# Kernel tuning notes

Hardware: AMD Instinct MI355X
Metric: run time of the kernel (lower is better)

The kernel has to match this reference:

```python
import jax, jax.numpy as jnp
import numpy as np

B, T, L, D, S = 256, 64, 32, 128, 4


def setup_inputs() -> dict:
    key = jax.random.key(0)
    k0, k1, k2, k3, k4, k5 = jax.random.split(key, 6)
    X = jax.random.normal(k0, (B, T, D), jnp.float32)
    decoding_manifold_means = jax.random.normal(k1, (B, S, T, D), jnp.float32)
    R_diag = jax.random.uniform(k2, (D,), jnp.float32, 0.5, 1.5)
    encoding_mus = jax.random.normal(k3, (B, T, L), jnp.float32)
    # PSD per-latent posterior covariance blocks: Sigma = 0.01*A A^T + I
    A = jax.random.normal(k4, (B, L, T, T), jnp.float32) * 0.1
    Sig = A @ jnp.swapaxes(A, -1, -2) + jnp.eye(T, dtype=jnp.float32)  # [B,L,T,T]
    encoding_Sigmas = jnp.transpose(Sig, (0, 2, 3, 1))  # [B,T,T,L]
    # RBF GP prior kernel per latent with noise jitter (sde_kernel_matrices analogue)
    times = jnp.arange(T, dtype=jnp.float32)
    taus = jax.random.uniform(k5, (L,), jnp.float32, 2.0, 10.0)
    dt2 = (times[:, None] - times[None, :]) ** 2  # [T,T]
    signal_var, noise_var = 0.999, 1e-3
    K = signal_var * jnp.exp(-dt2[:, :, None] / (2.0 * taus[None, None, :] ** 2))
    K = K + noise_var * jnp.eye(T, dtype=jnp.float32)[:, :, None]  # [T,T,L]
    return {
        "X": X,
        "decoding_manifold_means": decoding_manifold_means,
        "R_diag": R_diag,
        "encoding_mus": encoding_mus,
        "encoding_Sigmas": encoding_Sigmas,
        "K": K,
    }


def _gpml_loss(X, decoding_manifold_means, R_diag, encoding_mus, encoding_Sigmas, K):
    Bx, Tt, Ld = encoding_mus.shape
    Dd = X.shape[-1]
    # ---- KL(q || prior), exploiting block-diagonal structure over latents ----
    Sig = jnp.transpose(encoding_Sigmas, (0, 3, 1, 2))  # [B,L,T,T]
    Kp = jnp.transpose(K, (2, 0, 1))                    # [L,T,T]
    Lk = jnp.linalg.cholesky(Kp)                        # [L,T,T]
    Ls = jnp.linalg.cholesky(Sig)                       # [B,L,T,T]
    logdet_K = 2.0 * jnp.sum(jnp.log(jnp.diagonal(Lk, axis1=-2, axis2=-1)), -1)  # [L]
    logdet_S = 2.0 * jnp.sum(jnp.log(jnp.diagonal(Ls, axis1=-2, axis2=-1)), -1)  # [B,L]
    # tr(K^-1 Sigma) = ||Lk^-1 Ls||_F^2
    M = jax.scipy.linalg.solve_triangular(Lk[None], Ls, lower=True)  # [B,L,T,T]
    trace_term = jnp.sum(M * M, axis=(-2, -1))                       # [B,L]
    mu = jnp.transpose(encoding_mus, (0, 2, 1))                      # [B,L,T]
    w = jax.scipy.linalg.solve_triangular(Lk[None], mu[..., None], lower=True)  # [B,L,T,1]
    maha = jnp.sum(w * w, axis=(-2, -1))                             # [B,L]
    kl = 0.5 * jnp.sum(logdet_K[None, :] - logdet_S - Tt + trace_term + maha, axis=1)  # [B]
    # ---- log-likelihood under diagonal-R Gaussian observation model ----
    diff = X[:, None, :, :] - decoding_manifold_means  # [B,S,T,D]
    log2pi = jnp.log(jnp.asarray(2.0 * np.pi, X.dtype))
    ll_t = -0.5 * (jnp.sum(diff * diff / R_diag, -1) + jnp.sum(jnp.log(R_diag)) + Dd * log2pi)  # [B,S,T]
    ll = jnp.sum(ll_t, axis=-1)  # [B,S] (ll_loss summed over time)
    # per-batch negative ELBO: KL minus mean sample log-likelihood
    return kl - jnp.mean(ll, axis=1)  # [B]


def reference(X, decoding_manifold_means, R_diag, encoding_mus, encoding_Sigmas, K):
    return _gpml_loss(X, decoding_manifold_means, R_diag, encoding_mus, encoding_Sigmas, K)
```

## Files before the change

kernel.cpp:

```cpp
#include <hip/hip_runtime.h>
#include <math.h>

#define BN 256
#define TN 64
#define LN 32
#define DN 128
#define SN 4
#define HN 32

#define LOG2PI 1.8378770664093453f

__device__ __forceinline__ float bcastf(float v, int lane) {
    return __builtin_bit_cast(float, __builtin_amdgcn_readlane(__builtin_bit_cast(int, v), lane));
}
__device__ __forceinline__ float bf_lo(unsigned m) { return __builtin_bit_cast(float, m << 16); }
__device__ __forceinline__ float bf_hi(unsigned m) { return __builtin_bit_cast(float, m & 0xFFFF0000u); }


__device__ __forceinline__ int chunk_pos(int q, int i) { return (q + i + (i >> 3)) & 7; }

template<int Q>
__device__ __forceinline__ void fillp(float (&r)[HN], const float* plane, int slot) {
    if constexpr (Q < 8) {
        const float4 v = *(const float4*)(plane + slot * 32 + chunk_pos(Q, slot) * 4);
        r[4 * Q + 0] = v.x; r[4 * Q + 1] = v.y;
        r[4 * Q + 2] = v.z; r[4 * Q + 3] = v.w;
        fillp<Q + 1>(r, plane, slot);
    }
}
template<int JBASE, int J4>
__device__ __forceinline__ void trace_half(const float (&r)[HN], const float* __restrict__ kp,
                                           float mu, float& tr, float& sm) {
    if constexpr (J4 < 8) {
        float4 kv = *(const float4*)(kp + 4 * J4);
        tr = fmaf(kv.x, r[4 * J4 + 0], tr); sm = fmaf(kv.x, bcastf(mu, JBASE + 4 * J4 + 0), sm);
        tr = fmaf(kv.y, r[4 * J4 + 1], tr); sm = fmaf(kv.y, bcastf(mu, JBASE + 4 * J4 + 1), sm);
        tr = fmaf(kv.z, r[4 * J4 + 2], tr); sm = fmaf(kv.z, bcastf(mu, JBASE + 4 * J4 + 2), sm);
        tr = fmaf(kv.w, r[4 * J4 + 3], tr); sm = fmaf(kv.w, bcastf(mu, JBASE + 4 * J4 + 3), sm);
        trace_half<JBASE, J4 + 1>(r, kp, mu, tr, sm);
    }
}

template<int K, int J>
__device__ __forceinline__ void c1_upd(float (&r1)[HN], float c) {
    if constexpr (J < HN) {
        r1[J] = fmaf(-c, bcastf(r1[K], J), r1[J]);
        c1_upd<K, J + 1>(r1, c);
    }
}
template<int K>
__device__ __forceinline__ void c1_sweep(float (&r1)[HN], unsigned (&m)[16], float& logdet) {
    if constexpr (K < HN) {
        float dkk = bcastf(r1[K], K);
        logdet += __logf(dkk);
        float c = r1[K] * __builtin_amdgcn_rcpf(dkk);
        c1_upd<K, K + 1>(r1, c);
        if constexpr (K & 1) m[K >> 1] |= (__builtin_bit_cast(unsigned, c) & 0xFFFF0000u);
        else                 m[K >> 1]  = (__builtin_bit_cast(unsigned, c) >> 16);
        c1_sweep<K + 1>(r1, m, logdet);
    }
}
template<int K, int J>
__device__ __forceinline__ void rep_upd(float (&r2)[HN], float c) {
    if constexpr (J < HN) {
        r2[J] = fmaf(-c, bcastf(r2[J], K), r2[J]);
        rep_upd<K, J + 1>(r2, c);
    }
}
template<int K>
__device__ __forceinline__ void rep_sweep(float (&r2)[HN], const unsigned (&m)[16]) {
    if constexpr (K < HN) {
        float c = (K & 1) ? bf_hi(m[K >> 1]) : bf_lo(m[K >> 1]);
        rep_upd<K, 0>(r2, c);
        rep_sweep<K + 1>(r2, m);
    }
}
template<int Q, int J>
__device__ __forceinline__ void solo_upd(float (&r2)[HN], float c) {
    if constexpr (J < HN) {
        r2[J] = fmaf(-c, bcastf(r2[Q], 32 + J), r2[J]);
        solo_upd<Q, J + 1>(r2, c);
    }
}
template<int Q>
__device__ __forceinline__ void solo_sweep(float (&r2)[HN], float& logdet) {
    if constexpr (Q < HN) {
        float dkk = bcastf(r2[Q], 32 + Q);
        logdet += __logf(dkk);
        float c = r2[Q] * __builtin_amdgcn_rcpf(dkk);
        solo_upd<Q, Q + 1>(r2, c);
        solo_sweep<Q + 1>(r2, logdet);
    }
}

__global__ __launch_bounds__(256)
void k_chol(const float* __restrict__ Sg,
            const float* __restrict__ mus,
            const float* __restrict__ kinv,
            const float* __restrict__ logdetK,
            float* __restrict__ out) {
    __shared__ float st[4 * 1024];

    int hw = blockIdx.x;
    int g = (hw & 7) * 256 + (hw >> 3);
    int b = g >> 3, lg = g & 7;

    int tid = threadIdx.x;
    int w = tid >> 6, lane = tid & 63;
    int l = lg * 4 + w;
    int slot = lane & 31;

    float mu = mus[((size_t)b * TN + lane) * LN + l];
    const float* kp = kinv + l * (TN * TN) + lane * TN;
    const float* plane = &st[w * 1024];

    auto stage = [&](int r0, int c0) {
#pragma unroll
        for (int it = 0; it < 4; ++it) {
            int m_ = tid + it * 256;
            int j = m_ & 31, i = m_ >> 5;
            const float* gp = Sg + ((((size_t)b * TN + r0 + i) * TN + c0 + j) * LN + lg * 4);
            float4 v = *(const float4*)gp;
            int off = i * 32 + chunk_pos(j >> 2, i) * 4 + (j & 3);
            st[0 * 1024 + off] = v.x;
            st[1 * 1024 + off] = v.y;
            st[2 * 1024 + off] = v.z;
            st[3 * 1024 + off] = v.w;
        }
    };

    float tr = 0.0f, sm = 0.0f, logdet = 0.0f;
    unsigned m[16];
    float r1[HN];

    stage(0, 0);
    __syncthreads();
    if (lane < 32) fillp<0>(r1, plane, slot);
    __syncthreads();
    stage(32, 0);
    __syncthreads();
    if (lane >= 32) fillp<0>(r1, plane, slot);

    trace_half<0, 0>(r1, kp, mu, tr, sm);
    c1_sweep<0>(r1, m, logdet);

    __syncthreads();
    float r2[HN];
    stage(0, 32);
    __syncthreads();
    if (lane < 32) fillp<0>(r2, plane, slot);
    __syncthreads();
    stage(32, 32);
    __syncthreads();
    if (lane >= 32) fillp<0>(r2, plane, slot);

    trace_half<32, 0>(r2, kp + 32, mu, tr, sm);
    rep_sweep<0>(r2, m);
    solo_sweep<0>(r2, logdet);

    float contrib = tr + mu * sm;
#pragma unroll
    for (int off = 32; off >= 1; off >>= 1) contrib += __shfl_xor(contrib, off, 64);

    if (lane == 0) {
        float klp = 0.5f * (logdetK[l] - logdet - (float)TN + contrib);
        atomicAdd(&out[b], klp);
    }
}

template<int J>
__device__ __forceinline__ void pan_load(float (&p)[HN], const float* __restrict__ Kmat,
                                         int i, int l, int jbase) {
    if constexpr (J < HN) {
        p[J] = Kmat[(i * TN + jbase + J) * LN + l];
        pan_load<J + 1>(p, Kmat, i, l, jbase);
    }
}
template<int K, int J>
__device__ __forceinline__ void ki_upd(float (&a)[HN], float c) {
    if constexpr (J < HN) {
        a[J] = fmaf(-c, bcastf(a[J], K), a[J]);
        ki_upd<K, J + 1>(a, c);
    }
}
template<int K>
__device__ __forceinline__ void ki_a1sweep(float (&a1)[HN], float& ld, float& piv, int i) {
    if constexpr (K < HN) {
        float dkk = bcastf(a1[K], K);
        ld += __logf(dkk);
        if (i == K) piv = dkk;
        float c = (i == K) ? 0.0f : a1[K] * __builtin_amdgcn_rcpf(dkk);
        ki_upd<K, K + 1>(a1, c);
        a1[K] = c;
        ki_a1sweep<K + 1>(a1, ld, piv, i);
    }
}
template<int K>
__device__ __forceinline__ void ki_replay(float (&a2)[HN], const float (&a1)[HN]) {
    if constexpr (K < HN) {
        ki_upd<K, 0>(a2, a1[K]);
        ki_replay<K + 1>(a2, a1);
    }
}
template<int Q, int J>
__device__ __forceinline__ void ki_upd2(float (&a2)[HN], float c) {
    if constexpr (J < HN) {
        a2[J] = fmaf(-c, bcastf(a2[J], 32 + Q), a2[J]);
        ki_upd2<Q, J + 1>(a2, c);
    }
}
template<int Q>
__device__ __forceinline__ void ki_a2sweep(float (&a2)[HN], float& ld, float& piv, int i) {
    if constexpr (Q < HN) {
        float dkk = bcastf(a2[Q], 32 + Q);
        ld += __logf(dkk);
        if (i == 32 + Q) piv = dkk;
        float c = (i == 32 + Q) ? 0.0f : a2[Q] * __builtin_amdgcn_rcpf(dkk);
        ki_upd2<Q, Q + 1>(a2, c);
        a2[Q] = c;
        ki_a2sweep<Q + 1>(a2, ld, piv, i);
    }
}
template<int J>
__device__ __forceinline__ void g1_init(float (&g)[HN], int i) {
    if constexpr (J < HN) { g[J] = (J == i) ? 1.0f : 0.0f; g1_init<J + 1>(g, i); }
}
template<int K, int J>
__device__ __forceinline__ void g1_updA(float (&g)[HN], float c) {
    if constexpr (J <= K) {
        g[J] = fmaf(-c, bcastf(g[J], K), g[J]);
        g1_updA<K, J + 1>(g, c);
    }
}
template<int K>
__device__ __forceinline__ void g1_phase1(float (&g)[HN], const float (&a1)[HN]) {
    if constexpr (K < HN) {
        g1_updA<K, 0>(g, a1[K]);
        g1_phase1<K + 1>(g, a1);
    }
}
template<int Q, int J>
__device__ __forceinline__ void g1_updB(float (&g)[HN], float c) {
    if constexpr (J < HN) {
        g[J] = fmaf(-c, bcastf(g[J], 32 + Q), g[J]);
        g1_updB<Q, J + 1>(g, c);
    }
}
template<int Q>
__device__ __forceinline__ void g1_phase2(float (&g)[HN], const float (&a2)[HN]) {
    if constexpr (Q < HN) {
        g1_updB<Q, 0>(g, a2[Q]);
        g1_phase2<Q + 1>(g, a2);
    }
}
template<int J>
__device__ __forceinline__ void g2_init(float (&g)[HN], int i) {
    if constexpr (J < HN) { g[J] = (32 + J == i) ? 1.0f : 0.0f; g2_init<J + 1>(g, i); }
}
template<int Q, int J>
__device__ __forceinline__ void g2_upd(float (&g)[HN], float c) {
    if constexpr (J <= Q) {
        g[J] = fmaf(-c, bcastf(g[J], 32 + Q), g[J]);
        g2_upd<Q, J + 1>(g, c);
    }
}
template<int Q>
__device__ __forceinline__ void g2_phase(float (&g)[HN], const float (&a2)[HN]) {
    if constexpr (Q < HN) {
        g2_upd<Q, 0>(g, a2[Q]);
        g2_phase<Q + 1>(g, a2);
    }
}
template<int J>
__device__ __forceinline__ void pan_out(const float (&g)[HN], float rdi,
                                        float* __restrict__ dst) {
    if constexpr (J < HN) {
        dst[J] = g[J] * rdi;
        pan_out<J + 1>(g, rdi, dst);
    }
}

__global__ __launch_bounds__(256)
void k_ll_kinv(const float* __restrict__ X,
               const float* __restrict__ Mn,
               const float* __restrict__ R,
               const float* __restrict__ Kmat,
               float* __restrict__ kinv,
               float* __restrict__ logdetK,
               float* __restrict__ out) {
    if (blockIdx.x < 64) {
        if (threadIdx.x >= 64) return;
        const int l = blockIdx.x >> 1;
        const int half = blockIdx.x & 1;
        const int i = threadIdx.x;

        float ld = 0.0f, piv = 1.0f;
        float a1[HN], a2[HN];
        pan_load<0>(a1, Kmat, i, l, 0);
        ki_a1sweep<0>(a1, ld, piv, i);
        pan_load<0>(a2, Kmat, i, l, 32);
        ki_replay<0>(a2, a1);
        ki_a2sweep<0>(a2, ld, piv, i);
        float rdi = __builtin_amdgcn_rcpf(piv);
        if (half == 0) {
            float g1[HN];
            g1_init<0>(g1, i);
            g1_phase1<0>(g1, a1);
            g1_phase2<0>(g1, a2);
            pan_out<0>(g1, rdi, kinv + l * (TN * TN) + i * TN);
        } else {
            float g2[HN];
            g2_init<0>(g2, i);
            g2_phase<0>(g2, a2);
            pan_out<0>(g2, rdi, kinv + l * (TN * TN) + i * TN + 32);
            if (i == 0) logdetK[l] = ld;
        }
        return;
    }

    int hw = blockIdx.x - 64;
    int g = (hw & 7) * 128 + (hw >> 3);
    int b = g >> 2, s = g & 3;
    int tid = threadIdx.x;

    const float4* xp = (const float4*)(X + (size_t)b * TN * DN);
    const float4* mp = (const float4*)(Mn + ((size_t)(b * SN + s) * TN) * DN);

    int c = tid & 31;
    float4 rv = ((const float4*)R)[c];
    float4 ri = make_float4(1.0f / rv.x, 1.0f / rv.y, 1.0f / rv.z, 1.0f / rv.w);

    float acc = 0.0f;
#pragma unroll
    for (int it = 0; it < (TN * DN / 4) / 256; ++it) {
        int f = tid + it * 256;
        float4 xv = xp[f];
        float4 mv = mp[f];
        float dx = xv.x - mv.x; acc = fmaf(dx * dx, ri.x, acc);
        float dy = xv.y - mv.y; acc = fmaf(dy * dy, ri.y, acc);
        float dz = xv.z - mv.z; acc = fmaf(dz * dz, ri.z, acc);
        float dw = xv.w - mv.w; acc = fmaf(dw * dw, ri.w, acc);
    }
#pragma unroll
    for (int off = 32; off >= 1; off >>= 1) acc += __shfl_xor(acc, off, 64);

    __shared__ float wsum[4];
    if ((tid & 63) == 0) wsum[tid >> 6] = acc;
    __syncthreads();
    if (tid == 0) {
        float q = wsum[0] + wsum[1] + wsum[2] + wsum[3];
        float val = q * (0.5f / SN);
        if (s == 0) {
            float slr = 0.0f;
#pragma unroll
            for (int d = 0; d < DN; ++d) slr += __logf(R[d]);
            val += 0.5f * (float)TN * (slr + (float)DN * LOG2PI);
        }
        atomicAdd(&out[b], val);
    }
}

extern "C" void kernel_launch(void* const* d_in, const int* in_sizes, int n_in,
                              void* d_out, int out_size, void* d_ws, size_t ws_size,
                              hipStream_t stream) {
    const float* X   = (const float*)d_in[0];
    const float* Mn  = (const float*)d_in[1];
    const float* R   = (const float*)d_in[2];
    const float* mus = (const float*)d_in[3];
    const float* Sg  = (const float*)d_in[4];
    const float* Km  = (const float*)d_in[5];
    float* out = (float*)d_out;

    float* kinv = (float*)d_ws;
    float* ldK  = kinv + LN * TN * TN;

    hipMemsetAsync(d_out, 0, BN * sizeof(float), stream);
    k_ll_kinv<<<64 + BN * SN, 256, 0, stream>>>(X, Mn, R, Km, kinv, ldK, out);
    k_chol<<<BN * 8, 256, 0, stream>>>(Sg, mus, kinv, ldK, out);
}
```

Before: 146.8 us.

## Broadcast pivot rows through LDS instead of per-element readlane in Cholesky sweeps

The Cholesky elimination used one v_readlane per element to broadcast the pivot row across the wavefront, which serialises through scalar registers. Now the pivot lane writes its row to a small LDS buffer and every lane reads it back as float4 loads, with wave barriers between steps. The mu values for the trace term are also staged in LDS instead of being broadcast by readlane. This trades many scalar readlane operations for LDS round trips and extra wave-level fences per pivot step, which add latency on a serial dependency chain.

Result: slower. 280.2 us (+90.9%).

```diff
diff --git a/kernel.cpp b/kernel.cpp
--- a/kernel.cpp
+++ b/kernel.cpp
@@ -15,6 +15,11 @@
 }
 __device__ __forceinline__ float bf_lo(unsigned m) { return __builtin_bit_cast(float, m << 16); }
 __device__ __forceinline__ float bf_hi(unsigned m) { return __builtin_bit_cast(float, m & 0xFFFF0000u); }
+
+__device__ __forceinline__ void wavefence() {
+    __builtin_amdgcn_wave_barrier();
+    asm volatile("" ::: "memory");
+}
 
 
 __device__ __forceinline__ int chunk_pos(int q, int i) { return (q + i + (i >> 3)) & 7; }
@@ -28,68 +33,92 @@
         fillp<Q + 1>(r, plane, slot);
     }
 }
-template<int JBASE, int J4>
-__device__ __forceinline__ void trace_half(const float (&r)[HN], const float* __restrict__ kp,
-                                           float mu, float& tr, float& sm) {
+template<int JB, int J4>
+__device__ __forceinline__ void trace_lds(const float (&r)[HN], const float* __restrict__ kp,
+                                          const float* mudp, float& tr, float& sm) {
     if constexpr (J4 < 8) {
         float4 kv = *(const float4*)(kp + 4 * J4);
-        tr = fmaf(kv.x, r[4 * J4 + 0], tr); sm = fmaf(kv.x, bcastf(mu, JBASE + 4 * J4 + 0), sm);
-        tr = fmaf(kv.y, r[4 * J4 + 1], tr); sm = fmaf(kv.y, bcastf(mu, JBASE + 4 * J4 + 1), sm);
-        tr = fmaf(kv.z, r[4 * J4 + 2], tr); sm = fmaf(kv.z, bcastf(mu, JBASE + 4 * J4 + 2), sm);
-        tr = fmaf(kv.w, r[4 * J4 + 3], tr); sm = fmaf(kv.w, bcastf(mu, JBASE + 4 * J4 + 3), sm);
-        trace_half<JBASE, J4 + 1>(r, kp, mu, tr, sm);
-    }
-}
-
-template<int K, int J>
-__device__ __forceinline__ void c1_upd(float (&r1)[HN], float c) {
-    if constexpr (J < HN) {
-        r1[J] = fmaf(-c, bcastf(r1[K], J), r1[J]);
-        c1_upd<K, J + 1>(r1, c);
-    }
-}
+        float4 mv = *(const float4*)(mudp + JB + 4 * J4);
+        tr = fmaf(kv.x, r[4 * J4 + 0], tr); sm = fmaf(kv.x, mv.x, sm);
+        tr = fmaf(kv.y, r[4 * J4 + 1], tr); sm = fmaf(kv.y, mv.y, sm);
+        tr = fmaf(kv.z, r[4 * J4 + 2], tr); sm = fmaf(kv.z, mv.z, sm);
+        tr = fmaf(kv.w, r[4 * J4 + 3], tr); sm = fmaf(kv.w, mv.w, sm);
+        trace_lds<JB, J4 + 1>(r, kp, mudp, tr, sm);
+    }
+}
+
+template<int QS>
+__device__ __forceinline__ void pub_write(const float (&r)[HN], float* pubp) {
+    if constexpr (QS < 8) {
+        *(float4*)(pubp + 4 * QS) = make_float4(r[4 * QS + 0], r[4 * QS + 1],
+                                                r[4 * QS + 2], r[4 * QS + 3]);
+        pub_write<QS + 1>(r, pubp);
+    }
+}
+template<int QS>
+__device__ __forceinline__ void row_fma(float (&r)[HN], float c, const float* pubp) {
+    if constexpr (QS < 8) {
+        float4 p = *(const float4*)(pubp + 4 * QS);
+        r[4 * QS + 0] = fmaf(-c, p.x, r[4 * QS + 0]);
+        r[4 * QS + 1] = fmaf(-c, p.y, r[4 * QS + 1]);
+        r[4 * QS + 2] = fmaf(-c, p.z, r[4 * QS + 2]);
+        r[4 * QS + 3] = fmaf(-c, p.w, r[4 * QS + 3]);
+        row_fma<QS + 1>(r, c, pubp);
+    }
+}
+
 template<int K>
-__device__ __forceinline__ void c1_sweep(float (&r1)[HN], unsigned (&m)[16], float& logdet) {
+__device__ __forceinline__ void p1_sweep(float (&r)[HN], unsigned (&m)[16],
+                                         float& logdet, float* pubp, int lane) {
     if constexpr (K < HN) {
-        float dkk = bcastf(r1[K], K);
-        logdet += __logf(dkk);
-        float c = r1[K] * __builtin_amdgcn_rcpf(dkk);
-        c1_upd<K, K + 1>(r1, c);
+        constexpr int CK = K >> 2, CE = K & 3;
+        if (lane == K) pub_write<CK>(r, pubp);
+        wavefence();
+        float4 pc = *(const float4*)(pubp + 4 * CK);
+        float d = (CE == 0) ? pc.x : (CE == 1) ? pc.y : (CE == 2) ? pc.z : pc.w;
+        logdet += __logf(d);
+        float c = r[K] * __builtin_amdgcn_rcpf(d);
+        r[4 * CK + 0] = fmaf(-c, pc.x, r[4 * CK + 0]);
+        r[4 * CK + 1] = fmaf(-c, pc.y, r[4 * CK + 1]);
+        r[4 * CK + 2] = fmaf(-c, pc.z, r[4 * CK + 2]);
+        r[4 * CK + 3] = fmaf(-c, pc.w, r[4 * CK + 3]);
+        row_fma<CK + 1>(r, c, pubp);
+        wavefence();
         if constexpr (K & 1) m[K >> 1] |= (__builtin_bit_cast(unsigned, c) & 0xFFFF0000u);
         else                 m[K >> 1]  = (__builtin_bit_cast(unsigned, c) >> 16);
-        c1_sweep<K + 1>(r1, m, logdet);
-    }
-}
-template<int K, int J>
-__device__ __forceinline__ void rep_upd(float (&r2)[HN], float c) {
-    if constexpr (J < HN) {
-        r2[J] = fmaf(-c, bcastf(r2[J], K), r2[J]);
-        rep_upd<K, J + 1>(r2, c);
+        p1_sweep<K + 1>(r, m, logdet, pubp, lane);
     }
 }
 template<int K>
-__device__ __forceinline__ void rep_sweep(float (&r2)[HN], const unsigned (&m)[16]) {
+__device__ __forceinline__ void p2_rep(float (&r)[HN], const unsigned (&m)[16],
+                                       float* pubp, int lane) {
     if constexpr (K < HN) {
+        if (lane == K) pub_write<0>(r, pubp);
+        wavefence();
         float c = (K & 1) ? bf_hi(m[K >> 1]) : bf_lo(m[K >> 1]);
-        rep_upd<K, 0>(r2, c);
-        rep_sweep<K + 1>(r2, m);
-    }
-}
-template<int Q, int J>
-__device__ __forceinline__ void solo_upd(float (&r2)[HN], float c) {
-    if constexpr (J < HN) {
-        r2[J] = fmaf(-c, bcastf(r2[Q], 32 + J), r2[J]);
-        solo_upd<Q, J + 1>(r2, c);
+        row_fma<0>(r, c, pubp);
+        wavefence();
+        p2_rep<K + 1>(r, m, pubp, lane);
     }
 }
 template<int Q>
-__device__ __forceinline__ void solo_sweep(float (&r2)[HN], float& logdet) {
+__device__ __forceinline__ void p2_solo(float (&r)[HN], float& logdet,
+                                        float* pubp, int lane) {
     if constexpr (Q < HN) {
-        float dkk = bcastf(r2[Q], 32 + Q);
-        logdet += __logf(dkk);
-        float c = r2[Q] * __builtin_amdgcn_rcpf(dkk);
-        solo_upd<Q, Q + 1>(r2, c);
-        solo_sweep<Q + 1>(r2, logdet);
+        constexpr int CQ = Q >> 2, CE = Q & 3;
+        if (lane == 32 + Q) pub_write<CQ>(r, pubp);
+        wavefence();
+        float4 pc = *(const float4*)(pubp + 4 * CQ);
+        float d = (CE == 0) ? pc.x : (CE == 1) ? pc.y : (CE == 2) ? pc.z : pc.w;
+        logdet += __logf(d);
+        float c = r[Q] * __builtin_amdgcn_rcpf(d);
+        r[4 * CQ + 0] = fmaf(-c, pc.x, r[4 * CQ + 0]);
+        r[4 * CQ + 1] = fmaf(-c, pc.y, r[4 * CQ + 1]);
+        r[4 * CQ + 2] = fmaf(-c, pc.z, r[4 * CQ + 2]);
+        r[4 * CQ + 3] = fmaf(-c, pc.w, r[4 * CQ + 3]);
+        row_fma<CQ + 1>(r, c, pubp);
+        wavefence();
+        p2_solo<Q + 1>(r, logdet, pubp, lane);
     }
 }
 
@@ -100,6 +129,8 @@
             const float* __restrict__ logdetK,
             float* __restrict__ out) {
     __shared__ float st[4 * 1024];
+    __shared__ float pubs[4 * 32];
+    __shared__ float muds[4 * 64];
 
     int hw = blockIdx.x;
     int g = (hw & 7) * 256 + (hw >> 3);
@@ -111,8 +142,11 @@
     int slot = lane & 31;
 
     float mu = mus[((size_t)b * TN + lane) * LN + l];
+    muds[w * 64 + lane] = mu;
     const float* kp = kinv + l * (TN * TN) + lane * TN;
     const float* plane = &st[w * 1024];
+    float* pubp = &pubs[w * 32];
+    const float* mudp = &muds[w * 64];
 
     auto stage = [&](int r0, int c0) {
 #pragma unroll
@@ -141,8 +175,8 @@
     __syncthreads();
     if (lane >= 32) fillp<0>(r1, plane, slot);
 
-    trace_half<0, 0>(r1, kp, mu, tr, sm);
-    c1_sweep<0>(r1, m, logdet);
+    trace_lds<0, 0>(r1, kp, mudp, tr, sm);
+    p1_sweep<0>(r1, m, logdet, pubp, lane);
 
     __syncthreads();
     float r2[HN];
@@ -154,9 +188,9 @@
     __syncthreads();
     if (lane >= 32) fillp<0>(r2, plane, slot);
 
-    trace_half<32, 0>(r2, kp + 32, mu, tr, sm);
-    rep_sweep<0>(r2, m);
-    solo_sweep<0>(r2, logdet);
+    trace_lds<32, 0>(r2, kp + 32, mudp, tr, sm);
+    p2_rep<0>(r2, m, pubp, lane);
+    p2_solo<0>(r2, logdet, pubp, lane);
 
     float contrib = tr + mu * sm;
 #pragma unroll
```

## Roll Cholesky sweeps into register-shifting loops and keep multipliers in LDS

Applied to the files above, without the earlier changes.

The fully unrolled template recursions for the in-register Cholesky elimination become partially unrolled runtime loops. Each step shifts the register row down by one, so every lane always reads `r1[0]`/`r2[0]` with a uniform, runtime-indexed readlane. The bf16-packed multipliers move from 16 registers into a per-lane LDS buffer with a rotated index, to cut register pressure and instruction footprint. In exchange, every step now does a full 31-wide update instead of a shrinking triangle, which roughly doubles the FMA/readlane count in the factor sweeps. It also adds LDS traffic.

After: 201.1 us. +37.0%, slower.

```diff
diff --git a/kernel.cpp b/kernel.cpp
--- a/kernel.cpp
+++ b/kernel.cpp
@@ -13,8 +13,6 @@
 __device__ __forceinline__ float bcastf(float v, int lane) {
     return __builtin_bit_cast(float, __builtin_amdgcn_readlane(__builtin_bit_cast(int, v), lane));
 }
-__device__ __forceinline__ float bf_lo(unsigned m) { return __builtin_bit_cast(float, m << 16); }
-__device__ __forceinline__ float bf_hi(unsigned m) { return __builtin_bit_cast(float, m & 0xFFFF0000u); }
 
 
 __device__ __forceinline__ int chunk_pos(int q, int i) { return (q + i + (i >> 3)) & 7; }
@@ -41,58 +39,6 @@
     }
 }
 
-template<int K, int J>
-__device__ __forceinline__ void c1_upd(float (&r1)[HN], float c) {
-    if constexpr (J < HN) {
-        r1[J] = fmaf(-c, bcastf(r1[K], J), r1[J]);
-        c1_upd<K, J + 1>(r1, c);
-    }
-}
-template<int K>
-__device__ __forceinline__ void c1_sweep(float (&r1)[HN], unsigned (&m)[16], float& logdet) {
-    if constexpr (K < HN) {
-        float dkk = bcastf(r1[K], K);
-        logdet += __logf(dkk);
-        float c = r1[K] * __builtin_amdgcn_rcpf(dkk);
-        c1_upd<K, K + 1>(r1, c);
-        if constexpr (K & 1) m[K >> 1] |= (__builtin_bit_cast(unsigned, c) & 0xFFFF0000u);
-        else                 m[K >> 1]  = (__builtin_bit_cast(unsigned, c) >> 16);
-        c1_sweep<K + 1>(r1, m, logdet);
-    }
-}
-template<int K, int J>
-__device__ __forceinline__ void rep_upd(float (&r2)[HN], float c) {
-    if constexpr (J < HN) {
-        r2[J] = fmaf(-c, bcastf(r2[J], K), r2[J]);
-        rep_upd<K, J + 1>(r2, c);
-    }
-}
-template<int K>
-__device__ __forceinline__ void rep_sweep(float (&r2)[HN], const unsigned (&m)[16]) {
-    if constexpr (K < HN) {
-        float c = (K & 1) ? bf_hi(m[K >> 1]) : bf_lo(m[K >> 1]);
-        rep_upd<K, 0>(r2, c);
-        rep_sweep<K + 1>(r2, m);
-    }
-}
-template<int Q, int J>
-__device__ __forceinline__ void solo_upd(float (&r2)[HN], float c) {
-    if constexpr (J < HN) {
-        r2[J] = fmaf(-c, bcastf(r2[Q], 32 + J), r2[J]);
-        solo_upd<Q, J + 1>(r2, c);
-    }
-}
-template<int Q>
-__device__ __forceinline__ void solo_sweep(float (&r2)[HN], float& logdet) {
-    if constexpr (Q < HN) {
-        float dkk = bcastf(r2[Q], 32 + Q);
-        logdet += __logf(dkk);
-        float c = r2[Q] * __builtin_amdgcn_rcpf(dkk);
-        solo_upd<Q, Q + 1>(r2, c);
-        solo_sweep<Q + 1>(r2, logdet);
-    }
-}
-
 __global__ __launch_bounds__(256)
 void k_chol(const float* __restrict__ Sg,
             const float* __restrict__ mus,
@@ -100,6 +46,7 @@
             const float* __restrict__ logdetK,
             float* __restrict__ out) {
     __shared__ float st[4 * 1024];
+    __shared__ unsigned short cp16[4 * 2048];
 
     int hw = blockIdx.x;
     int g = (hw & 7) * 256 + (hw >> 3);
@@ -113,6 +60,7 @@
     float mu = mus[((size_t)b * TN + lane) * LN + l];
     const float* kp = kinv + l * (TN * TN) + lane * TN;
     const float* plane = &st[w * 1024];
+    unsigned short* cpp = &cp16[w * 2048 + lane * 32];
 
     auto stage = [&](int r0, int c0) {
 #pragma unroll
@@ -130,7 +78,6 @@
     };
 
     float tr = 0.0f, sm = 0.0f, logdet = 0.0f;
-    unsigned m[16];
     float r1[HN];
 
     stage(0, 0);
@@ -142,7 +89,17 @@
     if (lane >= 32) fillp<0>(r1, plane, slot);
 
     trace_half<0, 0>(r1, kp, mu, tr, sm);
-    c1_sweep<0>(r1, m, logdet);
+
+#pragma unroll 2
+    for (int K = 0; K < HN; ++K) {
+        float d = bcastf(r1[0], K);
+        logdet += __logf(d);
+        float c = r1[0] * __builtin_amdgcn_rcpf(d);
+        cpp[(K + lane) & 31] = (unsigned short)(__builtin_bit_cast(unsigned, c) >> 16);
+#pragma unroll
+        for (int s = 1; s < HN; ++s)
+            r1[s - 1] = fmaf(-c, bcastf(r1[s], K), r1[s]);
+    }
 
     __syncthreads();
     float r2[HN];
@@ -155,8 +112,24 @@
     if (lane >= 32) fillp<0>(r2, plane, slot);
 
     trace_half<32, 0>(r2, kp + 32, mu, tr, sm);
-    rep_sweep<0>(r2, m);
-    solo_sweep<0>(r2, logdet);
+
+#pragma unroll 4
+    for (int K = 0; K < HN; ++K) {
+        float c = __builtin_bit_cast(float, (unsigned)cpp[(K + lane) & 31] << 16);
+#pragma unroll
+        for (int s = 0; s < HN; ++s)
+            r2[s] = fmaf(-c, bcastf(r2[s], K), r2[s]);
+    }
+
+#pragma unroll 2
+    for (int Q = 0; Q < HN; ++Q) {
+        float d = bcastf(r2[0], 32 + Q);
+        logdet += __logf(d);
+        float c = r2[0] * __builtin_amdgcn_rcpf(d);
+#pragma unroll
+        for (int s = 1; s < HN; ++s)
+            r2[s - 1] = fmaf(-c, bcastf(r2[s], 32 + Q), r2[s]);
+    }
 
     float contrib = tr + mu * sm;
 #pragma unroll
```
